# Kernel tuning notes

Hardware: AMD Instinct MI355X
Metric: run time of the kernel (lower is better)

## Reference

```python
import jax, jax.numpy as jnp
import numpy as np

VOCAB, HIDDEN, BATCH, T = 32000, 256, 16, 256


def setup_inputs() -> dict:
    key = jax.random.key(0)
    ks = jax.random.split(key, 8)
    s_in = 1.0 / np.sqrt(HIDDEN)  # torch nn.RNN init scale (1/sqrt(hidden))
    inputs = jax.random.randint(ks[0], (BATCH, T), 0, VOCAB)
    targets = jax.random.randint(ks[1], (BATCH, T), 0, VOCAB)
    # RNN params: torch stores W_ih as (hidden, vocab); we keep the transpose
    # (vocab, hidden) so one_hot(x) @ W_ih.T == Wih[x] (an exact gather).
    Wih = jax.random.uniform(ks[2], (VOCAB, HIDDEN), minval=-s_in, maxval=s_in)
    bih = jax.random.uniform(ks[3], (HIDDEN,), minval=-s_in, maxval=s_in)
    Whh = jax.random.uniform(ks[4], (HIDDEN, HIDDEN), minval=-s_in, maxval=s_in)
    bhh = jax.random.uniform(ks[5], (HIDDEN,), minval=-s_in, maxval=s_in)
    Wfc = jax.random.uniform(ks[6], (VOCAB, HIDDEN), minval=-s_in, maxval=s_in)
    bfc = jax.random.uniform(ks[7], (VOCAB,), minval=-s_in, maxval=s_in)
    return {"inputs": inputs, "targets": targets, "Wih": Wih, "bih": bih,
            "Whh": Whh, "bhh": bhh, "Wfc": Wfc, "bfc": bfc}


def reference(inputs, targets, Wih, bih, Whh, bhh, Wfc, bfc):
    # one_hot(inputs) @ W_ih.T + b_ih  ==  Wih[inputs] + bih (exact same math)
    xproj = Wih[inputs] + bih                      # (B, T, H)
    B = inputs.shape[0]
    h0 = jnp.zeros((B, HIDDEN), dtype=Wih.dtype)

    def step(h, xt):
        h = jnp.tanh(xt + h @ Whh.T + bhh)
        return h, h

    _, hs = jax.lax.scan(step, h0, jnp.swapaxes(xproj, 0, 1))  # (T, B, H)
    hs = jnp.swapaxes(hs, 0, 1)                    # (B, T, H)
    logits = hs @ Wfc.T + bfc                      # (B, T, V)
    logp = jax.nn.log_softmax(logits, axis=-1)
    nll = -jnp.take_along_axis(logp, targets[..., None], axis=-1)
    return jnp.mean(nll)                           # scalar cross-entropy loss
```

## Files before the change

kernel.cpp:

```cpp
#include <hip/hip_runtime.h>
#include <hip/hip_bf16.h>
#include <stdint.h>

#define VOCAB 32000
#define HID   256
#define BATCH 16
#define SEQT  256
#define ROWS  (BATCH*SEQT)

typedef __attribute__((ext_vector_type(8))) short bf16x8_t;
typedef __attribute__((ext_vector_type(4))) float f32x4_t;

__device__ __forceinline__ short f2bs(float x) {
    __hip_bfloat16 h = __float2bfloat16(x);
    return *reinterpret_cast<short*>(&h);
}
__device__ __forceinline__ bf16x8_t cvt8(float4 a, float4 b) {
    union { short s[8]; bf16x8_t v; } u;
    u.s[0] = f2bs(a.x); u.s[1] = f2bs(a.y); u.s[2] = f2bs(a.z); u.s[3] = f2bs(a.w);
    u.s[4] = f2bs(b.x); u.s[5] = f2bs(b.y); u.s[6] = f2bs(b.z); u.s[7] = f2bs(b.w);
    return u.v;
}
__device__ __forceinline__ void barrier_lds() {
    asm volatile("s_waitcnt lgkmcnt(0)\n\ts_barrier" ::: "memory");
}
__device__ __forceinline__ float tanh_exp(float x) {
    float e = __builtin_amdgcn_exp2f(x * 2.885390081777927f);
    return fmaf(-2.f, __builtin_amdgcn_rcpf(e + 1.f), 1.f);
}
__device__ __forceinline__ uint32_t pk_bf16(float lo, float hi) {
    uint32_t r;
    asm("v_cvt_pk_bf16_f32 %0, %1, %2" : "=v"(r) : "v"(lo), "v"(hi));
    return r;
}
__device__ __forceinline__ void gload_lds16(const short* g, short* lds_base) {
    __builtin_amdgcn_global_load_lds(
        (const __attribute__((address_space(1))) void*)g,
        (__attribute__((address_space(3))) void*)lds_base, 16, 0, 0);
}


__global__ __launch_bounds__(256) void xproj_kernel(
    const int* __restrict__ inputs,
    const float* __restrict__ Wih,
    const float* __restrict__ bih,
    const float* __restrict__ bhh,
    const float* __restrict__ Wfc,
    float* __restrict__ xp,
    float* __restrict__ S,
    __hip_bfloat16* __restrict__ Wfcb,
    int do_cvt)
{
    int idx = blockIdx.x * 256 + threadIdx.x;
    int h  = idx & 255;
    int tb = idx >> 8;
    int b  = tb & 15;
    int t  = tb >> 4;
    int id = inputs[b * SEQT + t];
    xp[idx] = Wih[(size_t)id * HID + h] + bih[h] + bhh[h];
    if (idx < ROWS) S[idx] = 0.0f;
    if (do_cvt && idx < (VOCAB * HID / 8)) {
        int e   = idx * 8;
        int m   = (e >> 3) & 15;
        int lhh = (e >> 7) & 3;
        int ki  = (e >> 9) & 7;
        int tile = e >> 12;
        const float4* p = (const float4*)(Wfc + (size_t)(tile * 16 + m) * HID
                                          + ki * 32 + lhh * 8);
        *(bf16x8_t*)((short*)Wfcb + (size_t)e) = cvt8(p[0], p[1]);
    }
}

__global__ __launch_bounds__(256, 1) void rnn_kernel(
    const float* __restrict__ xp,
    const float* __restrict__ Whh,
    __hip_bfloat16* __restrict__ hs)
{
    __shared__ __align__(16) short hbuf[2][16][264];
    const int tid = threadIdx.x;
    const int l = tid & 63, w = tid >> 6;
    const int lr = l & 15, lh = l >> 4;
    const int n0 = w * 64 + lr * 4;
    short* hsg = (short*)hs + ((n0 >> 5) * 512) + (((n0 >> 3) & 3) * 128) + (n0 & 7);

    bf16x8_t bfrag[4][8];
#pragma unroll
    for (int c = 0; c < 4; c++)
#pragma unroll
        for (int ki = 0; ki < 8; ki++) {
            const float4* p = (const float4*)(Whh + (size_t)(n0 + c) * HID + ki * 32 + lh * 8);
            bfrag[c][ki] = cvt8(p[0], p[1]);
        }
    for (int i = tid; i < 16 * 264; i += 256) ((short*)hbuf[0])[i] = 0;
    __syncthreads();

    float4 xv[4], xw[4];
#pragma unroll
    for (int r = 0; r < 4; r++)
        xv[r] = *(const float4*)(xp + (lh * 4 + r) * HID + n0);

    auto step = [&](int SRC, int DST, float4* xc, float4* xn, int t) {
        bf16x8_t afr[8];
#pragma unroll
        for (int ki = 0; ki < 8; ki++)
            afr[ki] = *(const bf16x8_t*)(&hbuf[SRC][lr][ki * 32 + lh * 8]);

        f32x4_t A0 = {xc[0].x, xc[1].x, xc[2].x, xc[3].x};
        f32x4_t A1 = {xc[0].y, xc[1].y, xc[2].y, xc[3].y};
        f32x4_t A2 = {xc[0].z, xc[1].z, xc[2].z, xc[3].z};
        f32x4_t A3 = {xc[0].w, xc[1].w, xc[2].w, xc[3].w};
        f32x4_t B0 = {0,0,0,0}, B1 = {0,0,0,0}, B2 = {0,0,0,0}, B3 = {0,0,0,0};
#pragma unroll
        for (int ki = 0; ki < 4; ki++) {
            A0 = __builtin_amdgcn_mfma_f32_16x16x32_bf16(afr[ki],     bfrag[0][ki],     A0, 0, 0, 0);
            B0 = __builtin_amdgcn_mfma_f32_16x16x32_bf16(afr[ki + 4], bfrag[0][ki + 4], B0, 0, 0, 0);
            A1 = __builtin_amdgcn_mfma_f32_16x16x32_bf16(afr[ki],     bfrag[1][ki],     A1, 0, 0, 0);
            B1 = __builtin_amdgcn_mfma_f32_16x16x32_bf16(afr[ki + 4], bfrag[1][ki + 4], B1, 0, 0, 0);
            A2 = __builtin_amdgcn_mfma_f32_16x16x32_bf16(afr[ki],     bfrag[2][ki],     A2, 0, 0, 0);
            B2 = __builtin_amdgcn_mfma_f32_16x16x32_bf16(afr[ki + 4], bfrag[2][ki + 4], B2, 0, 0, 0);
            A3 = __builtin_amdgcn_mfma_f32_16x16x32_bf16(afr[ki],     bfrag[3][ki],     A3, 0, 0, 0);
            B3 = __builtin_amdgcn_mfma_f32_16x16x32_bf16(afr[ki + 4], bfrag[3][ki + 4], B3, 0, 0, 0);
        }

        if (t + 1 < SEQT) {
            const float* xb = xp + (size_t)(t + 1) * (BATCH * HID);
#pragma unroll
            for (int r = 0; r < 4; r++)
                xn[r] = *(const float4*)(xb + (lh * 4 + r) * HID + n0);
        }

#pragma unroll
        for (int r = 0; r < 4; r++) {
            float v0 = A0[r] + B0[r];
            float v1 = A1[r] + B1[r];
            float v2 = A2[r] + B2[r];
            float v3 = A3[r] + B3[r];
            uint2 u;
            u.x = pk_bf16(tanh_exp(v0), tanh_exp(v1));
            u.y = pk_bf16(tanh_exp(v2), tanh_exp(v3));
            *(uint2*)(&hbuf[DST][lh * 4 + r][n0]) = u;
            *(uint2*)(hsg + (size_t)t * 4096 + (lh * 4 + r) * 8) = u;
        }
        barrier_lds();
    };

    for (int t = 0; t < SEQT; t += 2) {
        step(0, 1, xv, xw, t);
        step(1, 0, xw, xv, t + 1);
    }
}

template <bool BF16B>
__global__ __launch_bounds__(256) void fc_kernel(
    const __hip_bfloat16* __restrict__ hsz,
    const void* __restrict__ WfcP,
    const float* __restrict__ bfc,
    const int* __restrict__ targets,
    float* __restrict__ S,
    float* __restrict__ TL)
{
    __shared__ __align__(16) short As[2][8 * 512];
    __shared__ __align__(16) short Bs[2][8 * 512];
    __shared__ int tgt[128];

    const int bid = blockIdx.x;
    const int xcd = bid & 7;
    const int j   = bid >> 3;
    const int m_id = j & 31;
    const int n_id = (j >> 5) * 8 + xcd;
    if (n_id >= VOCAB / 128) return;
    const int m0 = m_id * 128, n0 = n_id * 128;

    const int tid = threadIdx.x;
    const int l = tid & 63, w = tid >> 6;
    const int lr = l & 15, lh = l >> 4;
    const int wm = (w >> 1) * 64, wn = (w & 1) * 64;

    if (tid < 128) {
        int r = m0 + tid;
        tgt[tid] = targets[((r & 15) << 8) | (r >> 4)];
    }
    __builtin_amdgcn_sched_barrier(0);

    const short* Ag = (const short*)hsz + (size_t)m_id * 32768 + (size_t)(w * 2) * 4096 + l * 8;
    const short* Bg = (const short*)WfcP + (size_t)n_id * 32768 + (size_t)(w * 2) * 4096 + l * 8;
    const float* Bf = (const float*)WfcP;

    f32x4_t acc[4][4];
    const f32x4_t z = {0.f, 0.f, 0.f, 0.f};
#pragma unroll
    for (int i = 0; i < 4; i++)
#pragma unroll
        for (int jj = 0; jj < 4; jj++) acc[i][jj] = z;

    if (BF16B) {
        auto stage = [&](int buf, int s) {
            gload_lds16(Ag + s * 512,        &As[buf][(w * 2) * 512]);
            gload_lds16(Ag + 4096 + s * 512, &As[buf][(w * 2 + 1) * 512]);
            gload_lds16(Bg + s * 512,        &Bs[buf][(w * 2) * 512]);
            gload_lds16(Bg + 4096 + s * 512, &Bs[buf][(w * 2 + 1) * 512]);
        };
        stage(0, 0);
        stage(1, 1);
        __builtin_amdgcn_sched_barrier(0);

#pragma unroll
        for (int s = 0; s < 8; s++) {
            const int buf = s & 1;
            if (s < 7) asm volatile("s_waitcnt vmcnt(4)\n\ts_barrier" ::: "memory");
            else       asm volatile("s_waitcnt vmcnt(0)\n\ts_barrier" ::: "memory");

            bf16x8_t a[4], b[4];
#pragma unroll
            for (int mt = 0; mt < 4; mt++)
                a[mt] = *(const bf16x8_t*)&As[buf][(((w >> 1) * 4 + mt) * 512) + l * 8];
#pragma unroll
            for (int nt = 0; nt < 4; nt++)
                b[nt] = *(const bf16x8_t*)&Bs[buf][(((w & 1) * 4 + nt) * 512) + l * 8];

            if (s < 6) {
                barrier_lds();
                stage(buf, s + 2);
                __builtin_amdgcn_sched_barrier(0);
            }
#pragma unroll
            for (int mt = 0; mt < 4; mt++)
#pragma unroll
                for (int nt = 0; nt < 4; nt++)
                    acc[mt][nt] = __builtin_amdgcn_mfma_f32_16x16x32_bf16(
                        a[mt], b[nt], acc[mt][nt], 0, 0, 0);
        }
    } else {
        for (int s = 0; s < 8; s++) {
            __syncthreads();
#pragma unroll
            for (int i = 0; i < 2; i++) {
                int tt = w * 2 + i;
                bf16x8_t va = *(const bf16x8_t*)(Ag + i * 4096 + s * 512);
                *(bf16x8_t*)&As[0][tt * 512 + l * 8] = va;
                int n = n0 + tt * 16 + lr;
                const float4* p = (const float4*)(Bf + (size_t)n * HID + s * 32 + lh * 8);
                *(bf16x8_t*)&Bs[0][tt * 512 + l * 8] = cvt8(p[0], p[1]);
            }
            __syncthreads();
            bf16x8_t a[4], b[4];
#pragma unroll
            for (int mt = 0; mt < 4; mt++)
                a[mt] = *(const bf16x8_t*)&As[0][(((w >> 1) * 4 + mt) * 512) + l * 8];
#pragma unroll
            for (int nt = 0; nt < 4; nt++)
                b[nt] = *(const bf16x8_t*)&Bs[0][(((w & 1) * 4 + nt) * 512) + l * 8];
#pragma unroll
            for (int mt = 0; mt < 4; mt++)
#pragma unroll
                for (int nt = 0; nt < 4; nt++)
                    acc[mt][nt] = __builtin_amdgcn_mfma_f32_16x16x32_bf16(
                        a[mt], b[nt], acc[mt][nt], 0, 0, 0);
        }
    }

    int tg[16];
#pragma unroll
    for (int i = 0; i < 16; i++)
        tg[i] = tgt[wm + (i >> 2) * 16 + lh * 4 + (i & 3)];

    float rsum[16];
#pragma unroll
    for (int i = 0; i < 16; i++) rsum[i] = 0.f;
#pragma unroll
    for (int nt = 0; nt < 4; nt++) {
        int n = n0 + wn + nt * 16 + lr;
        float bias = bfc[n];
#pragma unroll
        for (int mt = 0; mt < 4; mt++)
#pragma unroll
            for (int r = 0; r < 4; r++) {
                float v = acc[mt][nt][r] + bias;
                rsum[mt * 4 + r] += __expf(v);
                if (tg[mt * 4 + r] == n)
                    TL[m0 + wm + mt * 16 + lh * 4 + r] = v;
            }
    }
#pragma unroll
    for (int m = 1; m < 16; m <<= 1)
#pragma unroll
        for (int i = 0; i < 16; i++) rsum[i] += __shfl_xor(rsum[i], m, 64);
    if (lr == 0) {
#pragma unroll
        for (int i = 0; i < 16; i++) {
            int r = m0 + wm + (i >> 2) * 16 + lh * 4 + (i & 3);
            atomicAdd(&S[r], rsum[i]);
        }
    }
}

__global__ __launch_bounds__(256) void loss_kernel(
    const float* __restrict__ S,
    const float* __restrict__ TL,
    float* __restrict__ out)
{
    int tid = threadIdx.x;
    float p = 0.f;
    for (int i = tid; i < ROWS; i += 256) p += __logf(S[i]) - TL[i];
#pragma unroll
    for (int m = 1; m < 64; m <<= 1) p += __shfl_xor(p, m, 64);
    __shared__ float red[4];
    if ((tid & 63) == 0) red[tid >> 6] = p;
    __syncthreads();
    if (tid == 0)
        out[0] = (red[0] + red[1] + red[2] + red[3]) / (float)ROWS;
}

extern "C" void kernel_launch(void* const* d_in, const int* in_sizes, int n_in,
                              void* d_out, int out_size, void* d_ws, size_t ws_size,
                              hipStream_t stream)
{
    (void)in_sizes; (void)n_in; (void)out_size;
    const int*   inputs  = (const int*)d_in[0];
    const int*   targets = (const int*)d_in[1];
    const float* Wih = (const float*)d_in[2];
    const float* bih = (const float*)d_in[3];
    const float* Whh = (const float*)d_in[4];
    const float* bhh = (const float*)d_in[5];
    const float* Wfc = (const float*)d_in[6];
    const float* bfc = (const float*)d_in[7];

    float* S  = (float*)d_ws;
    float* TL = S + ROWS;
    float* xp = TL + ROWS;
    __hip_bfloat16* hs = (__hip_bfloat16*)(xp + (size_t)SEQT * BATCH * HID);
    __hip_bfloat16* Wfcb = hs + (size_t)ROWS * HID;

    const size_t need = (size_t)(2 * ROWS) * 4 + (size_t)ROWS * HID * 4
                      + (size_t)ROWS * HID * 2 + (size_t)VOCAB * HID * 2;
    const int use_bf16b = (ws_size >= need) ? 1 : 0;

    xproj_kernel<<<(SEQT * BATCH * HID) / 256, 256, 0, stream>>>(
        inputs, Wih, bih, bhh, Wfc, xp, S, Wfcb, use_bf16b);
    rnn_kernel<<<1, 256, 0, stream>>>(xp, Whh, hs);
    if (use_bf16b)
        fc_kernel<true><<<8192, 256, 0, stream>>>(hs, (const void*)Wfcb, bfc, targets, S, TL);
    else
        fc_kernel<false><<<8192, 256, 0, stream>>>(hs, (const void*)Wfc, bfc, targets, S, TL);
    loss_kernel<<<1, 256, 0, stream>>>(S, TL, (float*)d_out);
}
```

Before: 470.7 us.

## Fuse RNN and FC into one cooperative kernel with progress-flag overlap

```diff
diff --git a/kernel.cpp b/kernel.cpp
--- a/kernel.cpp
+++ b/kernel.cpp
@@ -7,6 +7,9 @@
 #define BATCH 16
 #define SEQT  256
 #define ROWS  (BATCH*SEQT)
+
+#define NWORKERS 255
+#define NTILES   (32*125)
 
 typedef __attribute__((ext_vector_type(8))) short bf16x8_t;
 typedef __attribute__((ext_vector_type(4))) float f32x4_t;
@@ -49,6 +52,7 @@
     float* __restrict__ xp,
     float* __restrict__ S,
     __hip_bfloat16* __restrict__ Wfcb,
+    int* __restrict__ prog,
     int do_cvt)
 {
     int idx = blockIdx.x * 256 + threadIdx.x;
@@ -59,95 +63,246 @@
     int id = inputs[b * SEQT + t];
     xp[idx] = Wih[(size_t)id * HID + h] + bih[h] + bhh[h];
     if (idx < ROWS) S[idx] = 0.0f;
-    if (do_cvt && idx < (VOCAB * HID / 8)) {
-        int e   = idx * 8;
-        int m   = (e >> 3) & 15;
-        int lhh = (e >> 7) & 3;
-        int ki  = (e >> 9) & 7;
-        int tile = e >> 12;
-        const float4* p = (const float4*)(Wfc + (size_t)(tile * 16 + m) * HID
-                                          + ki * 32 + lhh * 8);
-        *(bf16x8_t*)((short*)Wfcb + (size_t)e) = cvt8(p[0], p[1]);
-    }
-}
-
-__global__ __launch_bounds__(256, 1) void rnn_kernel(
+    if (do_cvt) {
+        if (idx == 0) prog[0] = -1;
+        if (idx < (VOCAB * HID / 8)) {
+            int e   = idx * 8;
+            int m   = (e >> 3) & 15;
+            int lhh = (e >> 7) & 3;
+            int ki  = (e >> 9) & 7;
+            int tile = e >> 12;
+            const float4* p = (const float4*)(Wfc + (size_t)(tile * 16 + m) * HID
+                                              + ki * 32 + lhh * 8);
+            *(bf16x8_t*)((short*)Wfcb + (size_t)e) = cvt8(p[0], p[1]);
+        }
+    }
+}
+
+__device__ void rnn_core(const float* __restrict__ xp,
+                         const float* __restrict__ Whh,
+                         __hip_bfloat16* __restrict__ hs,
+                         int* __restrict__ prog)
+{
+    __shared__ __align__(8) short hbuf[2][16][264];
+    const int tid = threadIdx.x;
+    const int l = tid & 63, w = tid >> 6;
+    const int lr = l & 15, lh = l >> 4;
+    const int n0 = w * 32 + lr * 2;
+    short* hsg = (short*)hs + (n0 >> 5) * 512 + (((n0 >> 3) & 3) * 128) + (n0 & 7);
+
+    bf16x8_t bfrag[2][8];
+#pragma unroll
+    for (int nt = 0; nt < 2; nt++)
+#pragma unroll
+        for (int ki = 0; ki < 8; ki++) {
+            const float4* p = (const float4*)(Whh + (size_t)(n0 + nt) * HID + ki * 32 + lh * 8);
+            bfrag[nt][ki] = cvt8(p[0], p[1]);
+        }
+    for (int i = tid; i < 16 * 264; i += 512) ((short*)hbuf[0])[i] = 0;
+    __syncthreads();
+
+    float2 xva[4], xvb[4];
+#pragma unroll
+    for (int r = 0; r < 4; r++)
+        xva[r] = *(const float2*)(xp + (lh * 4 + r) * HID + n0);
+
+    auto step = [&](int SRC, int DST, float2* xc, float2* xn, int t) {
+        bf16x8_t afr[8];
+#pragma unroll
+        for (int ki = 0; ki < 8; ki++)
+            afr[ki] = *(const bf16x8_t*)(&hbuf[SRC][lr][ki * 32 + lh * 8]);
+
+        f32x4_t a0a = {xc[0].x, xc[1].x, xc[2].x, xc[3].x};
+        f32x4_t a1a = {xc[0].y, xc[1].y, xc[2].y, xc[3].y};
+        f32x4_t a0b = {0.f, 0.f, 0.f, 0.f};
+        f32x4_t a1b = {0.f, 0.f, 0.f, 0.f};
+#pragma unroll
+        for (int ki = 0; ki < 4; ki++) {
+            a0a = __builtin_amdgcn_mfma_f32_16x16x32_bf16(afr[ki],     bfrag[0][ki],     a0a, 0, 0, 0);
+            a0b = __builtin_amdgcn_mfma_f32_16x16x32_bf16(afr[ki + 4], bfrag[0][ki + 4], a0b, 0, 0, 0);
+            a1a = __builtin_amdgcn_mfma_f32_16x16x32_bf16(afr[ki],     bfrag[1][ki],     a1a, 0, 0, 0);
+            a1b = __builtin_amdgcn_mfma_f32_16x16x32_bf16(afr[ki + 4], bfrag[1][ki + 4], a1b, 0, 0, 0);
+        }
+
+        if (t + 1 < SEQT) {
+            const float* xb = xp + (size_t)(t + 1) * (BATCH * HID);
+#pragma unroll
+            for (int r = 0; r < 4; r++)
+                xn[r] = *(const float2*)(xb + (lh * 4 + r) * HID + n0);
+        }
+
+#pragma unroll
+        for (int r = 0; r < 4; r++) {
+            float v0 = a0a[r] + a0b[r];
+            float v1 = a1a[r] + a1b[r];
+            uint32_t pk = pk_bf16(tanh_exp(v0), tanh_exp(v1));
+            *(uint32_t*)(&hbuf[DST][lh * 4 + r][n0]) = pk;
+            __hip_atomic_store((uint32_t*)(hsg + (size_t)t * 4096 + (lh * 4 + r) * 8),
+                               pk, __ATOMIC_RELAXED, __HIP_MEMORY_SCOPE_AGENT);
+        }
+        const bool pub = (prog != nullptr) && t && ((t & 7) == 0);
+        if (pub) asm volatile("s_waitcnt vmcnt(8)" ::: "memory");
+        barrier_lds();
+        if (pub && tid == 0)
+            __hip_atomic_store(prog, t - 1, __ATOMIC_RELAXED, __HIP_MEMORY_SCOPE_AGENT);
+    };
+
+    for (int t = 0; t < SEQT; t += 2) {
+        step(0, 1, xva, xvb, t);
+        step(1, 0, xvb, xva, t + 1);
+    }
+    if (prog != nullptr) {
+        asm volatile("s_waitcnt vmcnt(0)" ::: "memory");
+        __syncthreads();
+        if (tid == 0)
+            __hip_atomic_store(prog, SEQT - 1, __ATOMIC_RELAXED, __HIP_MEMORY_SCOPE_AGENT);
+    }
+}
+
+__device__ void fc_worker(
+    const __hip_bfloat16* __restrict__ hsz,
+    const __hip_bfloat16* __restrict__ Wfcb,
+    const float* __restrict__ bfc,
+    const int* __restrict__ targets,
+    float* __restrict__ S,
+    float* __restrict__ TL,
+    int* __restrict__ prog,
+    int wid)
+{
+    __shared__ __align__(16) short As[2][8][512];
+    __shared__ __align__(16) short Bs[2][16][512];
+    __shared__ int tgt[128];
+
+    const int tid = threadIdx.x;
+    const int l = tid & 63, w = tid >> 6;
+    const int lr = l & 15, lh = l >> 4;
+    const int wm = (w >> 2) * 64, wn = (w & 3) * 64;
+
+    for (int ti = wid; ti < NTILES; ti += NWORKERS) {
+        const int m_id = ti / 125;
+        const int n2   = ti - m_id * 125;
+        const int m0 = m_id * 128, n0 = n2 * 256;
+
+        if (tid == 0) {
+            const int need = m_id * 8 + 7;
+            int spin = 0;
+            while (__hip_atomic_load(prog, __ATOMIC_RELAXED, __HIP_MEMORY_SCOPE_AGENT) < need) {
+                __builtin_amdgcn_s_sleep(4);
+                if (++spin > (1 << 18)) break;
+            }
+            __builtin_amdgcn_fence(__ATOMIC_ACQUIRE, "agent");
+        }
+        __syncthreads();
+
+        if (tid < 128) {
+            int r = m0 + tid;
+            tgt[tid] = targets[((r & 15) << 8) | (r >> 4)];
+        }
+        __builtin_amdgcn_sched_barrier(0);
+
+        const short* Ag = (const short*)hsz  + (size_t)(m_id * 8 + w)  * 4096 + l * 8;
+        const short* Bg = (const short*)Wfcb + (size_t)(n2 * 16 + 2*w) * 4096 + l * 8;
+
+        f32x4_t acc[4][4];
+        const f32x4_t z = {0.f, 0.f, 0.f, 0.f};
+#pragma unroll
+        for (int i = 0; i < 4; i++)
+#pragma unroll
+            for (int jj = 0; jj < 4; jj++) acc[i][jj] = z;
+
+        auto stage = [&](int buf, int s) {
+            gload_lds16(Ag + s * 512,        &As[buf][w][0]);
+            gload_lds16(Bg + s * 512,        &Bs[buf][2 * w][0]);
+            gload_lds16(Bg + 4096 + s * 512, &Bs[buf][2 * w + 1][0]);
+        };
+        stage(0, 0);
+        stage(1, 1);
+        __builtin_amdgcn_sched_barrier(0);
+
+#pragma unroll
+        for (int s = 0; s < 8; s++) {
+            const int buf = s & 1;
+            if (s < 7) asm volatile("s_waitcnt vmcnt(3)\n\ts_barrier" ::: "memory");
+            else       asm volatile("s_waitcnt vmcnt(0)\n\ts_barrier" ::: "memory");
+
+            bf16x8_t a[4], b[4];
+#pragma unroll
+            for (int mt = 0; mt < 4; mt++)
+                a[mt] = *(const bf16x8_t*)&As[buf][(w >> 2) * 4 + mt][l * 8];
+#pragma unroll
+            for (int nt = 0; nt < 4; nt++)
+                b[nt] = *(const bf16x8_t*)&Bs[buf][(w & 3) * 4 + nt][l * 8];
+
+            if (s < 6) {
+                barrier_lds();
+                stage(buf, s + 2);
+                __builtin_amdgcn_sched_barrier(0);
+            }
+#pragma unroll
+            for (int mt = 0; mt < 4; mt++)
+#pragma unroll
+                for (int nt = 0; nt < 4; nt++)
+                    acc[mt][nt] = __builtin_amdgcn_mfma_f32_16x16x32_bf16(
+                        a[mt], b[nt], acc[mt][nt], 0, 0, 0);
+        }
+
+        int tg[16];
+#pragma unroll
+        for (int i = 0; i < 16; i++)
+            tg[i] = tgt[wm + (i >> 2) * 16 + lh * 4 + (i & 3)];
+
+        float rsum[16];
+#pragma unroll
+        for (int i = 0; i < 16; i++) rsum[i] = 0.f;
+#pragma unroll
+        for (int nt = 0; nt < 4; nt++) {
+            int n = n0 + wn + nt * 16 + lr;
+            float bias = bfc[n];
+#pragma unroll
+            for (int mt = 0; mt < 4; mt++)
+#pragma unroll
+                for (int r = 0; r < 4; r++) {
+                    float v = acc[mt][nt][r] + bias;
+                    rsum[mt * 4 + r] += __expf(v);
+                    if (tg[mt * 4 + r] == n)
+                        TL[m0 + wm + mt * 16 + lh * 4 + r] = v;
+                }
+        }
+#pragma unroll
+        for (int m = 1; m < 16; m <<= 1)
+#pragma unroll
+            for (int i = 0; i < 16; i++) rsum[i] += __shfl_xor(rsum[i], m, 64);
+        if (lr == 0) {
+#pragma unroll
+            for (int i = 0; i < 16; i++) {
+                int r = m0 + wm + (i >> 2) * 16 + lh * 4 + (i & 3);
+                atomicAdd(&S[r], rsum[i]);
+            }
+        }
+    }
+}
+
+__global__ __launch_bounds__(512, 1) void rnnfc_kernel(
+    const float* __restrict__ xp,
+    const float* __restrict__ Whh,
+    __hip_bfloat16* __restrict__ hs,
+    const __hip_bfloat16* __restrict__ Wfcb,
+    const float* __restrict__ bfc,
+    const int* __restrict__ targets,
+    float* __restrict__ S,
+    float* __restrict__ TL,
+    int* __restrict__ prog)
+{
+    if (blockIdx.x == 0) rnn_core(xp, Whh, hs, prog);
+    else                 fc_worker(hs, Wfcb, bfc, targets, S, TL, prog, (int)blockIdx.x - 1);
+}
+
+__global__ __launch_bounds__(512, 1) void rnn_kernel(
     const float* __restrict__ xp,
     const float* __restrict__ Whh,
     __hip_bfloat16* __restrict__ hs)
 {
-    __shared__ __align__(16) short hbuf[2][16][264];
-    const int tid = threadIdx.x;
-    const int l = tid & 63, w = tid >> 6;
-    const int lr = l & 15, lh = l >> 4;
-    const int n0 = w * 64 + lr * 4;
-    short* hsg = (short*)hs + ((n0 >> 5) * 512) + (((n0 >> 3) & 3) * 128) + (n0 & 7);
-
-    bf16x8_t bfrag[4][8];
-#pragma unroll
-    for (int c = 0; c < 4; c++)
-#pragma unroll
-        for (int ki = 0; ki < 8; ki++) {
-            const float4* p = (const float4*)(Whh + (size_t)(n0 + c) * HID + ki * 32 + lh * 8);
-            bfrag[c][ki] = cvt8(p[0], p[1]);
-        }
-    for (int i = tid; i < 16 * 264; i += 256) ((short*)hbuf[0])[i] = 0;
-    __syncthreads();
-
-    float4 xv[4], xw[4];
-#pragma unroll
-    for (int r = 0; r < 4; r++)
-        xv[r] = *(const float4*)(xp + (lh * 4 + r) * HID + n0);
-
-    auto step = [&](int SRC, int DST, float4* xc, float4* xn, int t) {
-        bf16x8_t afr[8];
-#pragma unroll
-        for (int ki = 0; ki < 8; ki++)
-            afr[ki] = *(const bf16x8_t*)(&hbuf[SRC][lr][ki * 32 + lh * 8]);
-
-        f32x4_t A0 = {xc[0].x, xc[1].x, xc[2].x, xc[3].x};
-        f32x4_t A1 = {xc[0].y, xc[1].y, xc[2].y, xc[3].y};
-        f32x4_t A2 = {xc[0].z, xc[1].z, xc[2].z, xc[3].z};
-        f32x4_t A3 = {xc[0].w, xc[1].w, xc[2].w, xc[3].w};
-        f32x4_t B0 = {0,0,0,0}, B1 = {0,0,0,0}, B2 = {0,0,0,0}, B3 = {0,0,0,0};
-#pragma unroll
-        for (int ki = 0; ki < 4; ki++) {
-            A0 = __builtin_amdgcn_mfma_f32_16x16x32_bf16(afr[ki],     bfrag[0][ki],     A0, 0, 0, 0);
-            B0 = __builtin_amdgcn_mfma_f32_16x16x32_bf16(afr[ki + 4], bfrag[0][ki + 4], B0, 0, 0, 0);
-            A1 = __builtin_amdgcn_mfma_f32_16x16x32_bf16(afr[ki],     bfrag[1][ki],     A1, 0, 0, 0);
-            B1 = __builtin_amdgcn_mfma_f32_16x16x32_bf16(afr[ki + 4], bfrag[1][ki + 4], B1, 0, 0, 0);
-            A2 = __builtin_amdgcn_mfma_f32_16x16x32_bf16(afr[ki],     bfrag[2][ki],     A2, 0, 0, 0);
-            B2 = __builtin_amdgcn_mfma_f32_16x16x32_bf16(afr[ki + 4], bfrag[2][ki + 4], B2, 0, 0, 0);
-            A3 = __builtin_amdgcn_mfma_f32_16x16x32_bf16(afr[ki],     bfrag[3][ki],     A3, 0, 0, 0);
-            B3 = __builtin_amdgcn_mfma_f32_16x16x32_bf16(afr[ki + 4], bfrag[3][ki + 4], B3, 0, 0, 0);
-        }
-
-        if (t + 1 < SEQT) {
-            const float* xb = xp + (size_t)(t + 1) * (BATCH * HID);
-#pragma unroll
-            for (int r = 0; r < 4; r++)
-                xn[r] = *(const float4*)(xb + (lh * 4 + r) * HID + n0);
-        }
-
-#pragma unroll
-        for (int r = 0; r < 4; r++) {
-            float v0 = A0[r] + B0[r];
-            float v1 = A1[r] + B1[r];
-            float v2 = A2[r] + B2[r];
-            float v3 = A3[r] + B3[r];
-            uint2 u;
-            u.x = pk_bf16(tanh_exp(v0), tanh_exp(v1));
-            u.y = pk_bf16(tanh_exp(v2), tanh_exp(v3));
-            *(uint2*)(&hbuf[DST][lh * 4 + r][n0]) = u;
-            *(uint2*)(hsg + (size_t)t * 4096 + (lh * 4 + r) * 8) = u;
-        }
-        barrier_lds();
-    };
-
-    for (int t = 0; t < SEQT; t += 2) {
-        step(0, 1, xv, xw, t);
-        step(1, 0, xw, xv, t + 1);
-    }
+    rnn_core(xp, Whh, hs, nullptr);
 }
 
 template <bool BF16B>
@@ -330,17 +485,29 @@
     float* xp = TL + ROWS;
     __hip_bfloat16* hs = (__hip_bfloat16*)(xp + (size_t)SEQT * BATCH * HID);
     __hip_bfloat16* Wfcb = hs + (size_t)ROWS * HID;
+    int* prog = (int*)(Wfcb + (size_t)VOCAB * HID);
 
     const size_t need = (size_t)(2 * ROWS) * 4 + (size_t)ROWS * HID * 4
-                      + (size_t)ROWS * HID * 2 + (size_t)VOCAB * HID * 2;
+                      + (size_t)ROWS * HID * 2 + (size_t)VOCAB * HID * 2 + 256;
     const int use_bf16b = (ws_size >= need) ? 1 : 0;
 
     xproj_kernel<<<(SEQT * BATCH * HID) / 256, 256, 0, stream>>>(
-        inputs, Wih, bih, bhh, Wfc, xp, S, Wfcb, use_bf16b);
-    rnn_kernel<<<1, 256, 0, stream>>>(xp, Whh, hs);
-    if (use_bf16b)
-        fc_kernel<true><<<8192, 256, 0, stream>>>(hs, (const void*)Wfcb, bfc, targets, S, TL);
-    else
-        fc_kernel<false><<<8192, 256, 0, stream>>>(hs, (const void*)Wfc, bfc, targets, S, TL);
+        inputs, Wih, bih, bhh, Wfc, xp, S, Wfcb, prog, use_bf16b);
+
+    bool fused_ok = false;
+    if (use_bf16b) {
+        void* ka[] = {(void*)&xp, (void*)&Whh, (void*)&hs, (void*)&Wfcb,
+                      (void*)&bfc, (void*)&targets, (void*)&S, (void*)&TL, (void*)&prog};
+        hipError_t e = hipLaunchCooperativeKernel((const void*)rnnfc_kernel,
+                                                  dim3(256), dim3(512), ka, 0, stream);
+        fused_ok = (e == hipSuccess);
+    }
+    if (!fused_ok) {
+        rnn_kernel<<<1, 512, 0, stream>>>(xp, Whh, hs);
+        if (use_bf16b)
+            fc_kernel<true><<<8192, 256, 0, stream>>>(hs, (const void*)Wfcb, bfc, targets, S, TL);
+        else
+            fc_kernel<false><<<8192, 256, 0, stream>>>(hs, (const void*)Wfc, bfc, targets, S, TL);
+    }
     loss_kernel<<<1, 256, 0, stream>>>(S, TL, (float*)d_out);
 }
```

Measured after the change: 1.302 ms. 176% more time.

## Overlap Wfc bf16 conversion with RNN recurrence and widen RNN block to 8 waves

Applied to the files above, without the earlier changes.

```diff
diff --git a/kernel.cpp b/kernel.cpp
--- a/kernel.cpp
+++ b/kernel.cpp
@@ -45,11 +45,8 @@
     const float* __restrict__ Wih,
     const float* __restrict__ bih,
     const float* __restrict__ bhh,
-    const float* __restrict__ Wfc,
     float* __restrict__ xp,
-    float* __restrict__ S,
-    __hip_bfloat16* __restrict__ Wfcb,
-    int do_cvt)
+    float* __restrict__ S)
 {
     int idx = blockIdx.x * 256 + threadIdx.x;
     int h  = idx & 255;
@@ -59,7 +56,89 @@
     int id = inputs[b * SEQT + t];
     xp[idx] = Wih[(size_t)id * HID + h] + bih[h] + bhh[h];
     if (idx < ROWS) S[idx] = 0.0f;
-    if (do_cvt && idx < (VOCAB * HID / 8)) {
+}
+
+__device__ void rnn_core(const float* __restrict__ xp,
+                         const float* __restrict__ Whh,
+                         __hip_bfloat16* __restrict__ hs)
+{
+    __shared__ __align__(8) short hbuf[2][16][264];
+    const int tid = threadIdx.x;
+    const int l = tid & 63, w = tid >> 6;
+    const int lr = l & 15, lh = l >> 4;
+    const int n0 = w * 32 + lr * 2;
+    short* hsg = (short*)hs + (n0 >> 5) * 512 + (((n0 >> 3) & 3) * 128) + (n0 & 7);
+
+    bf16x8_t bfrag[2][8];
+#pragma unroll
+    for (int nt = 0; nt < 2; nt++)
+#pragma unroll
+        for (int ki = 0; ki < 8; ki++) {
+            const float4* p = (const float4*)(Whh + (size_t)(n0 + nt) * HID + ki * 32 + lh * 8);
+            bfrag[nt][ki] = cvt8(p[0], p[1]);
+        }
+    for (int i = tid; i < 16 * 264; i += 512) ((short*)hbuf[0])[i] = 0;
+    __syncthreads();
+
+    float2 xva[4], xvb[4];
+#pragma unroll
+    for (int r = 0; r < 4; r++)
+        xva[r] = *(const float2*)(xp + (lh * 4 + r) * HID + n0);
+
+    auto step = [&](int SRC, int DST, float2* xc, float2* xn, int t) {
+        bf16x8_t afr[8];
+#pragma unroll
+        for (int ki = 0; ki < 8; ki++)
+            afr[ki] = *(const bf16x8_t*)(&hbuf[SRC][lr][ki * 32 + lh * 8]);
+
+        f32x4_t a0a = {xc[0].x, xc[1].x, xc[2].x, xc[3].x};
+        f32x4_t a1a = {xc[0].y, xc[1].y, xc[2].y, xc[3].y};
+        f32x4_t a0b = {0.f, 0.f, 0.f, 0.f};
+        f32x4_t a1b = {0.f, 0.f, 0.f, 0.f};
+#pragma unroll
+        for (int ki = 0; ki < 4; ki++) {
+            a0a = __builtin_amdgcn_mfma_f32_16x16x32_bf16(afr[ki],     bfrag[0][ki],     a0a, 0, 0, 0);
+            a0b = __builtin_amdgcn_mfma_f32_16x16x32_bf16(afr[ki + 4], bfrag[0][ki + 4], a0b, 0, 0, 0);
+            a1a = __builtin_amdgcn_mfma_f32_16x16x32_bf16(afr[ki],     bfrag[1][ki],     a1a, 0, 0, 0);
+            a1b = __builtin_amdgcn_mfma_f32_16x16x32_bf16(afr[ki + 4], bfrag[1][ki + 4], a1b, 0, 0, 0);
+        }
+
+        if (t + 1 < SEQT) {
+            const float* xb = xp + (size_t)(t + 1) * (BATCH * HID);
+#pragma unroll
+            for (int r = 0; r < 4; r++)
+                xn[r] = *(const float2*)(xb + (lh * 4 + r) * HID + n0);
+        }
+
+#pragma unroll
+        for (int r = 0; r < 4; r++) {
+            float v0 = a0a[r] + a0b[r];
+            float v1 = a1a[r] + a1b[r];
+            uint32_t pk = pk_bf16(tanh_exp(v0), tanh_exp(v1));
+            *(uint32_t*)(&hbuf[DST][lh * 4 + r][n0]) = pk;
+            *(uint32_t*)(hsg + (size_t)t * 4096 + (lh * 4 + r) * 8) = pk;
+        }
+        barrier_lds();
+    };
+
+    for (int t = 0; t < SEQT; t += 2) {
+        step(0, 1, xva, xvb, t);
+        step(1, 0, xvb, xva, t + 1);
+    }
+}
+
+__global__ __launch_bounds__(512, 1) void rnncvt_kernel(
+    const float* __restrict__ xp,
+    const float* __restrict__ Whh,
+    __hip_bfloat16* __restrict__ hs,
+    const float* __restrict__ Wfc,
+    __hip_bfloat16* __restrict__ Wfcb,
+    int do_cvt)
+{
+    if (blockIdx.x == 0) { rnn_core(xp, Whh, hs); return; }
+    if (!do_cvt) return;
+    for (int idx = (int)(blockIdx.x - 1) * 512 + threadIdx.x;
+         idx < (VOCAB * HID / 8); idx += 256 * 512) {
         int e   = idx * 8;
         int m   = (e >> 3) & 15;
         int lhh = (e >> 7) & 3;
@@ -68,85 +147,6 @@
         const float4* p = (const float4*)(Wfc + (size_t)(tile * 16 + m) * HID
                                           + ki * 32 + lhh * 8);
         *(bf16x8_t*)((short*)Wfcb + (size_t)e) = cvt8(p[0], p[1]);
-    }
-}
-
-__global__ __launch_bounds__(256, 1) void rnn_kernel(
-    const float* __restrict__ xp,
-    const float* __restrict__ Whh,
-    __hip_bfloat16* __restrict__ hs)
-{
-    __shared__ __align__(16) short hbuf[2][16][264];
-    const int tid = threadIdx.x;
-    const int l = tid & 63, w = tid >> 6;
-    const int lr = l & 15, lh = l >> 4;
-    const int n0 = w * 64 + lr * 4;
-    short* hsg = (short*)hs + ((n0 >> 5) * 512) + (((n0 >> 3) & 3) * 128) + (n0 & 7);
-
-    bf16x8_t bfrag[4][8];
-#pragma unroll
-    for (int c = 0; c < 4; c++)
-#pragma unroll
-        for (int ki = 0; ki < 8; ki++) {
-            const float4* p = (const float4*)(Whh + (size_t)(n0 + c) * HID + ki * 32 + lh * 8);
-            bfrag[c][ki] = cvt8(p[0], p[1]);
-        }
-    for (int i = tid; i < 16 * 264; i += 256) ((short*)hbuf[0])[i] = 0;
-    __syncthreads();
-
-    float4 xv[4], xw[4];
-#pragma unroll
-    for (int r = 0; r < 4; r++)
-        xv[r] = *(const float4*)(xp + (lh * 4 + r) * HID + n0);
-
-    auto step = [&](int SRC, int DST, float4* xc, float4* xn, int t) {
-        bf16x8_t afr[8];
-#pragma unroll
-        for (int ki = 0; ki < 8; ki++)
-            afr[ki] = *(const bf16x8_t*)(&hbuf[SRC][lr][ki * 32 + lh * 8]);
-
-        f32x4_t A0 = {xc[0].x, xc[1].x, xc[2].x, xc[3].x};
-        f32x4_t A1 = {xc[0].y, xc[1].y, xc[2].y, xc[3].y};
-        f32x4_t A2 = {xc[0].z, xc[1].z, xc[2].z, xc[3].z};
-        f32x4_t A3 = {xc[0].w, xc[1].w, xc[2].w, xc[3].w};
-        f32x4_t B0 = {0,0,0,0}, B1 = {0,0,0,0}, B2 = {0,0,0,0}, B3 = {0,0,0,0};
-#pragma unroll
-        for (int ki = 0; ki < 4; ki++) {
-            A0 = __builtin_amdgcn_mfma_f32_16x16x32_bf16(afr[ki],     bfrag[0][ki],     A0, 0, 0, 0);
-            B0 = __builtin_amdgcn_mfma_f32_16x16x32_bf16(afr[ki + 4], bfrag[0][ki + 4], B0, 0, 0, 0);
-            A1 = __builtin_amdgcn_mfma_f32_16x16x32_bf16(afr[ki],     bfrag[1][ki],     A1, 0, 0, 0);
-            B1 = __builtin_amdgcn_mfma_f32_16x16x32_bf16(afr[ki + 4], bfrag[1][ki + 4], B1, 0, 0, 0);
-            A2 = __builtin_amdgcn_mfma_f32_16x16x32_bf16(afr[ki],     bfrag[2][ki],     A2, 0, 0, 0);
-            B2 = __builtin_amdgcn_mfma_f32_16x16x32_bf16(afr[ki + 4], bfrag[2][ki + 4], B2, 0, 0, 0);
-            A3 = __builtin_amdgcn_mfma_f32_16x16x32_bf16(afr[ki],     bfrag[3][ki],     A3, 0, 0, 0);
-            B3 = __builtin_amdgcn_mfma_f32_16x16x32_bf16(afr[ki + 4], bfrag[3][ki + 4], B3, 0, 0, 0);
-        }
-
-        if (t + 1 < SEQT) {
-            const float* xb = xp + (size_t)(t + 1) * (BATCH * HID);
-#pragma unroll
-            for (int r = 0; r < 4; r++)
-                xn[r] = *(const float4*)(xb + (lh * 4 + r) * HID + n0);
-        }
-
-#pragma unroll
-        for (int r = 0; r < 4; r++) {
-            float v0 = A0[r] + B0[r];
-            float v1 = A1[r] + B1[r];
-            float v2 = A2[r] + B2[r];
-            float v3 = A3[r] + B3[r];
-            uint2 u;
-            u.x = pk_bf16(tanh_exp(v0), tanh_exp(v1));
-            u.y = pk_bf16(tanh_exp(v2), tanh_exp(v3));
-            *(uint2*)(&hbuf[DST][lh * 4 + r][n0]) = u;
-            *(uint2*)(hsg + (size_t)t * 4096 + (lh * 4 + r) * 8) = u;
-        }
-        barrier_lds();
-    };
-
-    for (int t = 0; t < SEQT; t += 2) {
-        step(0, 1, xv, xw, t);
-        step(1, 0, xw, xv, t + 1);
     }
 }
 
@@ -336,8 +336,8 @@
     const int use_bf16b = (ws_size >= need) ? 1 : 0;
 
     xproj_kernel<<<(SEQT * BATCH * HID) / 256, 256, 0, stream>>>(
-        inputs, Wih, bih, bhh, Wfc, xp, S, Wfcb, use_bf16b);
-    rnn_kernel<<<1, 256, 0, stream>>>(xp, Whh, hs);
+        inputs, Wih, bih, bhh, xp, S);
+    rnncvt_kernel<<<257, 512, 0, stream>>>(xp, Whh, hs, Wfc, Wfcb, use_bf16b);
     if (use_bf16b)
         fc_kernel<true><<<8192, 256, 0, stream>>>(hs, (const void*)Wfcb, bfc, targets, S, TL);
     else
```

Result: faster. 442.1 us (-6.1%).
